# Kernel optimization log

Measured on AMD Instinct MI355X. Metric: run time of the kernel, lower is better.

Reference implementation:

```python
import jax, jax.numpy as jnp
import numpy as np

IN_F = 2048
OUT_F = 2048
G = 5 + 3  # grid_size + spline_order
BATCH = 8192


def setup_inputs() -> dict:
    key = jax.random.key(0)
    k1, k2, k3 = jax.random.split(key, 3)
    x = jax.random.normal(k1, (BATCH, IN_F), dtype=jnp.float32)
    # kaiming_uniform(a=sqrt(5)) on (out,in): bound = 1/sqrt(in)
    bound = 1.0 / np.sqrt(IN_F)
    base_weight = jax.random.uniform(k2, (OUT_F, IN_F), dtype=jnp.float32,
                                     minval=-bound, maxval=bound)
    grid = 0.1 * jax.random.normal(k3, (IN_F, OUT_F, G), dtype=jnp.float32)
    return {"x": x, "base_weight": base_weight, "grid": grid}


def reference(x, base_weight, grid):
    # base branch: standard linear  (B, out)
    base_out = x @ base_weight.T
    # spline branch: Gaussian basis around the scalar grid mean  (B, in)
    basis = jnp.exp(-jnp.square(x - grid.mean()))
    # contract over in_features and the grid dim: sum_i sum_g basis[b,i]*grid[i,o,g]
    spline_out = basis @ grid.sum(axis=-1)  # (B, out)
    return base_out + spline_out
```

## Files before the change

### kernel.cpp

```cpp
#include <hip/hip_runtime.h>

#define IN_F   2048
#define OUT_F  2048
#define GDIM   8
#define BATCH  8192
#define KDIM   4096
#define GRID_TOTAL_INV (1.0f / 33554432.0f)

typedef __bf16 bf16x8 __attribute__((ext_vector_type(8)));
typedef float  f32x4  __attribute__((ext_vector_type(4)));
typedef unsigned short u16x8 __attribute__((ext_vector_type(8)));

__device__ __forceinline__ unsigned short f2bf(float f) {
  union { float f; unsigned int u; } v; v.f = f;
  unsigned int r = v.u + 0x7fffu + ((v.u >> 16) & 1u);
  return (unsigned short)(r >> 16);
}

__device__ __forceinline__ void gload_lds16(const void* g, void* l) {
  __builtin_amdgcn_global_load_lds(
      (const __attribute__((address_space(1))) void*)g,
      (__attribute__((address_space(3))) void*)l, 16, 0, 0);
}

__global__ __launch_bounds__(256) void prep_bw(const float* __restrict__ bw,
                                               unsigned short* __restrict__ Bt,
                                               float* __restrict__ sum_ptr) {
  if (blockIdx.x == 0 && threadIdx.x == 0) *sum_ptr = 0.0f;
  size_t i8 = ((size_t)blockIdx.x * 256 + threadIdx.x) * 8;
  const float4* p = reinterpret_cast<const float4*>(bw + i8);
  float4 a = p[0], b = p[1];
  u16x8 v;
  v[0] = f2bf(a.x); v[1] = f2bf(a.y); v[2] = f2bf(a.z); v[3] = f2bf(a.w);
  v[4] = f2bf(b.x); v[5] = f2bf(b.y); v[6] = f2bf(b.z); v[7] = f2bf(b.w);
  size_t o = i8 >> 11;
  size_t k = i8 & 2047;
  *reinterpret_cast<u16x8*>(Bt + o * KDIM + k) = v;
}

__global__ __launch_bounds__(256) void prep_grid(const float* __restrict__ grid,
                                                 unsigned short* __restrict__ Bt,
                                                 float* __restrict__ sum_ptr) {
  __shared__ float tile[32][33];
  __shared__ float wsum[4];
  int bi = blockIdx.x >> 6;
  int bo = blockIdx.x & 63;
  int i0 = bi << 5, o0 = bo << 5;
  int t = threadIdx.x;
  float local = 0.f;
#pragma unroll
  for (int p = 0; p < 4; ++p) {
    int li = t + 256 * p;
    int il = li >> 5, ol = li & 31;
    const float4* g4 = reinterpret_cast<const float4*>(
        grid + ((size_t)(i0 + il) * OUT_F + (size_t)(o0 + ol)) * GDIM);
    float4 a = g4[0], b = g4[1];
    float s = ((a.x + a.y) + (a.z + a.w)) + ((b.x + b.y) + (b.z + b.w));
    tile[il][ol] = s;
    local += s;
  }
#pragma unroll
  for (int off = 32; off >= 1; off >>= 1) local += __shfl_down(local, off, 64);
  int lane = t & 63, w = t >> 6;
  if (lane == 0) wsum[w] = local;
  __syncthreads();
#pragma unroll
  for (int p = 0; p < 4; ++p) {
    int li = t + 256 * p;
    int ol = li >> 5, il = li & 31;
    Bt[(size_t)(o0 + ol) * KDIM + IN_F + (i0 + il)] = f2bf(tile[il][ol]);
  }
  if (t == 0) atomicAdd(sum_ptr, (wsum[0] + wsum[1]) + (wsum[2] + wsum[3]));
}

__global__ __launch_bounds__(256) void prep_A(const float* __restrict__ x,
                                              const float* __restrict__ sum_ptr,
                                              unsigned short* __restrict__ Abuf) {
  float m = *sum_ptr * GRID_TOTAL_INV;
  size_t i8 = ((size_t)blockIdx.x * 256 + threadIdx.x) * 8;
  const float4* p = reinterpret_cast<const float4*>(x + i8);
  float4 a = p[0], b = p[1];
  float xs[8] = {a.x, a.y, a.z, a.w, b.x, b.y, b.z, b.w};
  u16x8 xv, bv;
#pragma unroll
  for (int j = 0; j < 8; ++j) {
    xv[j] = f2bf(xs[j]);
    float d = xs[j] - m;
    bv[j] = f2bf(__expf(-d * d));
  }
  size_t bi = i8 >> 11;
  size_t k  = i8 & 2047;
  *reinterpret_cast<u16x8*>(Abuf + bi * KDIM + k) = xv;
  *reinterpret_cast<u16x8*>(Abuf + bi * KDIM + IN_F + k) = bv;
}

__global__ __launch_bounds__(256) void gemm_kernel(
    const unsigned short* __restrict__ A,
    const unsigned short* __restrict__ B,
    float* __restrict__ C) {
  __shared__ unsigned short As[128 * 64];
  __shared__ unsigned short Bs[128 * 64];
  int bm = blockIdx.x & 63;
  int bn = blockIdx.x >> 6;
  int t = threadIdx.x;
  int lane = t & 63;
  int wid  = t >> 6;
  int wm = wid >> 1, wn = wid & 1;

  const f32x4 fzero = {0.f, 0.f, 0.f, 0.f};
  f32x4 acc[4][4];
#pragma unroll
  for (int m = 0; m < 4; ++m)
#pragma unroll
    for (int n = 0; n < 4; ++n) acc[m][n] = fzero;

  const size_t a_row0 = (size_t)bm * 128;
  const size_t b_row0 = (size_t)bn * 128;

  const int pbase = wid * 1024 + lane * 16;

  for (int step = 0; step < 64; ++step) {
    const int k0 = step * 64;
#pragma unroll
    for (int issue = 0; issue < 4; ++issue) {
      int p  = issue * 4096 + pbase;
      int r  = p >> 7;
      int cg = ((p >> 4) & 7) ^ (r & 7);
      gload_lds16(A + (a_row0 + r) * KDIM + k0 + cg * 8,
                  (char*)As + issue * 4096 + wid * 1024);
      gload_lds16(B + (b_row0 + r) * KDIM + k0 + cg * 8,
                  (char*)Bs + issue * 4096 + wid * 1024);
    }
    __syncthreads();
#pragma unroll
    for (int kk = 0; kk < 2; ++kk) {
      bf16x8 af[4], bfr[4];
#pragma unroll
      for (int m = 0; m < 4; ++m) {
        int r = wm * 64 + m * 16 + (lane & 15);
        int c = (kk * 4 + (lane >> 4)) ^ (r & 7);
        af[m] = *reinterpret_cast<const bf16x8*>((const char*)As + r * 128 + c * 16);
      }
#pragma unroll
      for (int n = 0; n < 4; ++n) {
        int r = wn * 64 + n * 16 + (lane & 15);
        int c = (kk * 4 + (lane >> 4)) ^ (r & 7);
        bfr[n] = *reinterpret_cast<const bf16x8*>((const char*)Bs + r * 128 + c * 16);
      }
#pragma unroll
      for (int m = 0; m < 4; ++m)
#pragma unroll
        for (int n = 0; n < 4; ++n)
          acc[m][n] = __builtin_amdgcn_mfma_f32_16x16x32_bf16(
              af[m], bfr[n], acc[m][n], 0, 0, 0);
    }
    __syncthreads();
  }

  int rg = lane >> 4, cc = lane & 15;
  size_t crow0 = (size_t)bm * 128 + wm * 64;
  size_t ccol0 = (size_t)bn * 128 + wn * 64;
#pragma unroll
  for (int m = 0; m < 4; ++m)
#pragma unroll
    for (int n = 0; n < 4; ++n)
#pragma unroll
      for (int rr = 0; rr < 4; ++rr) {
        size_t row = crow0 + (size_t)m * 16 + rg * 4 + rr;
        size_t col = ccol0 + (size_t)n * 16 + cc;
        C[row * OUT_F + col] = acc[m][n][rr];
      }
}

extern "C" void kernel_launch(void* const* d_in, const int* in_sizes, int n_in,
                              void* d_out, int out_size, void* d_ws, size_t ws_size,
                              hipStream_t stream) {
  const float* x    = (const float*)d_in[0];
  const float* bw   = (const float*)d_in[1];
  const float* grid = (const float*)d_in[2];
  float* out = (float*)d_out;

  unsigned short* Abuf = (unsigned short*)d_ws;
  unsigned short* Bt   = Abuf + (size_t)BATCH * KDIM;
  float* sum_ptr = (float*)(Bt + (size_t)OUT_F * KDIM);

  prep_bw  <<<(OUT_F * IN_F / 8) / 256, 256, 0, stream>>>(bw, Bt, sum_ptr);
  prep_grid<<<64 * 64,                  256, 0, stream>>>(grid, Bt, sum_ptr);
  prep_A   <<<(BATCH * IN_F / 8) / 256, 256, 0, stream>>>(x, sum_ptr, Abuf);
  gemm_kernel<<<64 * 16, 256, 0, stream>>>(Abuf, Bt, out);
}
```

Baseline: 459.7 us.

## Rewrite GEMM as 256x256 tile with 4-stage async LDS pipeline

```diff
diff --git a/kernel.cpp b/kernel.cpp
--- a/kernel.cpp
+++ b/kernel.cpp
@@ -7,6 +7,11 @@
 #define KDIM   4096
 #define GRID_TOTAL_INV (1.0f / 33554432.0f)
 
+#define BK     32
+#define NT     (KDIM / BK)
+#define SLOT   32768
+#define ATILE  16384
+
 typedef __bf16 bf16x8 __attribute__((ext_vector_type(8)));
 typedef float  f32x4  __attribute__((ext_vector_type(4)));
 typedef unsigned short u16x8 __attribute__((ext_vector_type(8)));
@@ -21,6 +26,14 @@
   __builtin_amdgcn_global_load_lds(
       (const __attribute__((address_space(1))) void*)g,
       (__attribute__((address_space(3))) void*)l, 16, 0, 0);
+}
+
+template<int VM>
+__device__ __forceinline__ void wait_vm() {
+  if constexpr (VM == 12)     asm volatile("s_waitcnt vmcnt(12)" ::: "memory");
+  else if constexpr (VM == 8) asm volatile("s_waitcnt vmcnt(8)"  ::: "memory");
+  else if constexpr (VM == 4) asm volatile("s_waitcnt vmcnt(4)"  ::: "memory");
+  else                        asm volatile("s_waitcnt vmcnt(0)"  ::: "memory");
 }
 
 __global__ __launch_bounds__(256) void prep_bw(const float* __restrict__ bw,
@@ -94,74 +107,79 @@
   *reinterpret_cast<u16x8*>(Abuf + bi * KDIM + IN_F + k) = bv;
 }
 
-__global__ __launch_bounds__(256) void gemm_kernel(
+__global__ __launch_bounds__(512, 2) void gemm_kernel(
     const unsigned short* __restrict__ A,
     const unsigned short* __restrict__ B,
     float* __restrict__ C) {
-  __shared__ unsigned short As[128 * 64];
-  __shared__ unsigned short Bs[128 * 64];
-  int bm = blockIdx.x & 63;
-  int bn = blockIdx.x >> 6;
-  int t = threadIdx.x;
-  int lane = t & 63;
-  int wid  = t >> 6;
-  int wm = wid >> 1, wn = wid & 1;
-
-  const f32x4 fzero = {0.f, 0.f, 0.f, 0.f};
-  f32x4 acc[4][4];
-#pragma unroll
-  for (int m = 0; m < 4; ++m)
-#pragma unroll
-    for (int n = 0; n < 4; ++n) acc[m][n] = fzero;
-
-  const size_t a_row0 = (size_t)bm * 128;
-  const size_t b_row0 = (size_t)bn * 128;
-
-  const int pbase = wid * 1024 + lane * 16;
-
-  for (int step = 0; step < 64; ++step) {
-    const int k0 = step * 64;
-#pragma unroll
-    for (int issue = 0; issue < 4; ++issue) {
-      int p  = issue * 4096 + pbase;
-      int r  = p >> 7;
-      int cg = ((p >> 4) & 7) ^ (r & 7);
-      gload_lds16(A + (a_row0 + r) * KDIM + k0 + cg * 8,
-                  (char*)As + issue * 4096 + wid * 1024);
-      gload_lds16(B + (b_row0 + r) * KDIM + k0 + cg * 8,
-                  (char*)Bs + issue * 4096 + wid * 1024);
-    }
-    __syncthreads();
-#pragma unroll
-    for (int kk = 0; kk < 2; ++kk) {
-      bf16x8 af[4], bfr[4];
-#pragma unroll
-      for (int m = 0; m < 4; ++m) {
-        int r = wm * 64 + m * 16 + (lane & 15);
-        int c = (kk * 4 + (lane >> 4)) ^ (r & 7);
-        af[m] = *reinterpret_cast<const bf16x8*>((const char*)As + r * 128 + c * 16);
-      }
-#pragma unroll
-      for (int n = 0; n < 4; ++n) {
-        int r = wn * 64 + n * 16 + (lane & 15);
-        int c = (kk * 4 + (lane >> 4)) ^ (r & 7);
-        bfr[n] = *reinterpret_cast<const bf16x8*>((const char*)Bs + r * 128 + c * 16);
-      }
-#pragma unroll
-      for (int m = 0; m < 4; ++m)
-#pragma unroll
-        for (int n = 0; n < 4; ++n)
-          acc[m][n] = __builtin_amdgcn_mfma_f32_16x16x32_bf16(
-              af[m], bfr[n], acc[m][n], 0, 0, 0);
-    }
-    __syncthreads();
-  }
-
-  int rg = lane >> 4, cc = lane & 15;
-  size_t crow0 = (size_t)bm * 128 + wm * 64;
-  size_t ccol0 = (size_t)bn * 128 + wn * 64;
-#pragma unroll
-  for (int m = 0; m < 4; ++m)
+  __shared__ __align__(16) char lds[4 * SLOT];
+  const int t    = threadIdx.x;
+  const int lane = t & 63;
+  const int wid  = t >> 6;
+  const int wm   = wid >> 2;
+  const int wn   = wid & 3;
+  const int bx = blockIdx.x;
+  const int bm = ((bx & 7) << 2) | ((bx >> 3) & 3);
+  const int bn = bx >> 5;
+
+  f32x4 acc[8][4] = {};
+
+  const unsigned short* aSrc = A + ((size_t)(bm * 256 + (t >> 2)) * KDIM) + (t & 3) * 8;
+  const unsigned short* bSrc = B + ((size_t)(bn * 256 + (t >> 2)) * KDIM) + (t & 3) * 8;
+  const int dstOff = t * 16;
+
+  const int aRd = (wm * 128 + (lane & 15)) * 64 + (lane >> 4) * 16;
+  const int bRd = (wn * 64  + (lane & 15)) * 64 + (lane >> 4) * 16;
+
+  auto STAGE = [&](int tile) {
+    const int slot = (tile & 3) * SLOT;
+    const unsigned short* a = aSrc + tile * BK;
+    const unsigned short* b = bSrc + tile * BK;
+    gload_lds16(a,                        lds + slot + dstOff);
+    gload_lds16(a + 128 * KDIM,           lds + slot + 8192 + dstOff);
+    gload_lds16(b,                        lds + slot + ATILE + dstOff);
+    gload_lds16(b + 128 * KDIM,           lds + slot + ATILE + 8192 + dstOff);
+  };
+
+  auto BODY = [&](int slotbase) {
+    __builtin_amdgcn_sched_barrier(0);
+    const char* sa = lds + slotbase + aRd;
+    const char* sb = lds + slotbase + ATILE + bRd;
+    bf16x8 af[8], bf[4];
+#pragma unroll
+    for (int m = 0; m < 8; ++m)
+      af[m] = *reinterpret_cast<const bf16x8*>(sa + m * 1024);
+#pragma unroll
+    for (int n = 0; n < 4; ++n)
+      bf[n] = *reinterpret_cast<const bf16x8*>(sb + n * 1024);
+    asm volatile("s_waitcnt lgkmcnt(0)" ::: "memory");
+    __builtin_amdgcn_sched_barrier(0);
+    __builtin_amdgcn_s_barrier();
+    __builtin_amdgcn_s_setprio(1);
+#pragma unroll
+    for (int m = 0; m < 8; ++m)
+#pragma unroll
+      for (int n = 0; n < 4; ++n)
+        acc[m][n] = __builtin_amdgcn_mfma_f32_16x16x32_bf16(af[m], bf[n], acc[m][n], 0, 0, 0);
+    __builtin_amdgcn_s_setprio(0);
+  };
+
+  STAGE(0); STAGE(1); STAGE(2);
+
+  for (int kt = 0; kt < NT - 3; ++kt) {
+    STAGE(kt + 3);
+    wait_vm<12>();
+    __builtin_amdgcn_s_barrier();
+    BODY((kt & 3) * SLOT);
+  }
+  wait_vm<8>(); __builtin_amdgcn_s_barrier(); BODY(((NT - 3) & 3) * SLOT);
+  wait_vm<4>(); __builtin_amdgcn_s_barrier(); BODY(((NT - 2) & 3) * SLOT);
+  wait_vm<0>(); __builtin_amdgcn_s_barrier(); BODY(((NT - 1) & 3) * SLOT);
+
+  const int rg = lane >> 4, cc = lane & 15;
+  const size_t crow0 = (size_t)bm * 256 + wm * 128;
+  const size_t ccol0 = (size_t)bn * 256 + wn * 64;
+#pragma unroll
+  for (int m = 0; m < 8; ++m)
 #pragma unroll
     for (int n = 0; n < 4; ++n)
 #pragma unroll
@@ -187,5 +205,5 @@
   prep_bw  <<<(OUT_F * IN_F / 8) / 256, 256, 0, stream>>>(bw, Bt, sum_ptr);
   prep_grid<<<64 * 64,                  256, 0, stream>>>(grid, Bt, sum_ptr);
   prep_A   <<<(BATCH * IN_F / 8) / 256, 256, 0, stream>>>(x, sum_ptr, Abuf);
-  gemm_kernel<<<64 * 16, 256, 0, stream>>>(Abuf, Bt, out);
-}
+  gemm_kernel<<<256, 512, 0, stream>>>(Abuf, Bt, out);
+}
```

After: 416.6 us. 9.4% less time.
